# Performance work log

Measured on AMD Instinct MI355X. Metric: run time of the kernel, lower is better.

The kernel has to match this reference:

```python
import jax, jax.numpy as jnp
import numpy as np

H = 4  # attention heads


def gat_layer(x, src, dst, W, a_src, a_dst, b, N):
    """PyG-style GATConv (concat=True, negative_slope=0.2, eval-mode dropout)."""
    h = (x @ W).reshape(N, H, -1)                       # [N,H,C]
    es = jnp.einsum('nhc,hc->nh', h, a_src)             # per-node src score
    ed = jnp.einsum('nhc,hc->nh', h, a_dst)             # per-node dst score
    e = jax.nn.leaky_relu(es[src] + ed[dst], negative_slope=0.2)  # [E,H]
    # segment softmax over incoming edges of each destination node
    emax = jax.ops.segment_max(e, dst, num_segments=N)
    ee = jnp.exp(e - emax[dst])
    denom = jax.ops.segment_sum(ee, dst, num_segments=N)
    alpha = ee / (denom[dst] + 1e-16)                   # [E,H]
    out = jax.ops.segment_sum(h[src] * alpha[..., None], dst, num_segments=N)
    return out.reshape(N, -1) + b                        # [N,H*C]


def setup_inputs() -> dict:
    key = jax.random.key(0)
    ks = jax.random.split(key, 13)
    N, E, D, Q = 50000, 800000, 256, 8
    HID, OUT = 256, 256
    Ch, Co = HID // H, OUT // H
    inp = {}
    inp['x'] = jax.random.normal(ks[0], (N, D), dtype=jnp.float32)
    inp['edge_index'] = jax.random.randint(ks[1], (2, E), 0, N, dtype=jnp.int64)
    inp['query_embedding'] = jax.random.normal(ks[2], (Q, OUT), dtype=jnp.float32)
    # layer 1: input_dim -> heads * (hidden_dim//heads)
    inp['W1'] = jax.random.normal(ks[3], (D, HID), dtype=jnp.float32) / np.sqrt(D).astype(np.float32)
    inp['a_src1'] = jax.random.normal(ks[4], (H, Ch), dtype=jnp.float32) / np.sqrt(Ch).astype(np.float32)
    inp['a_dst1'] = jax.random.normal(ks[5], (H, Ch), dtype=jnp.float32) / np.sqrt(Ch).astype(np.float32)
    inp['b1'] = jnp.zeros((HID,), dtype=jnp.float32)
    # layer 2: hidden_dim -> heads * (output_dim//heads)
    inp['W2'] = jax.random.normal(ks[6], (HID, OUT), dtype=jnp.float32) / np.sqrt(HID).astype(np.float32)
    inp['a_src2'] = jax.random.normal(ks[7], (H, Co), dtype=jnp.float32) / np.sqrt(Co).astype(np.float32)
    inp['a_dst2'] = jax.random.normal(ks[8], (H, Co), dtype=jnp.float32) / np.sqrt(Co).astype(np.float32)
    inp['b2'] = jnp.zeros((OUT,), dtype=jnp.float32)
    # node classifier over concat([query, node]) -> 1 (intended Linear(2*OUT, 1))
    inp['Wc'] = jax.random.normal(ks[9], (2 * OUT, 1), dtype=jnp.float32) / np.sqrt(2 * OUT).astype(np.float32)
    inp['bc'] = jnp.zeros((1,), dtype=jnp.float32)
    return inp


def reference(x, edge_index, query_embedding, W1, a_src1, a_dst1, b1,
              W2, a_src2, a_dst2, b2, Wc, bc):
    N = x.shape[0]
    loops = jnp.arange(N, dtype=edge_index.dtype)        # GATConv add_self_loops=True
    src = jnp.concatenate([edge_index[0], loops])
    dst = jnp.concatenate([edge_index[1], loops])
    h = jax.nn.relu(gat_layer(x, src, dst, W1, a_src1, a_dst1, b1, N))
    emb = gat_layer(h, src, dst, W2, a_src2, a_dst2, b2, N)  # [N, OUT]
    D = emb.shape[1]
    # scores[q,n] = Linear(concat(query[q], emb[n])) — computed without
    # materializing the [Q,N,2D] concat (identical math).
    q_part = query_embedding @ Wc[:D] + bc               # [Q,1]
    n_part = emb @ Wc[D:]                                # [N,1]
    node_scores = q_part[:, 0][:, None] + n_part[:, 0][None, :]  # [Q,N]
    return emb, node_scores
```

## Files before the change

kernel.cpp:

```cpp
#include <hip/hip_runtime.h>

typedef unsigned short u16;
typedef unsigned int   u32;
typedef __attribute__((ext_vector_type(8))) short short8v;
typedef __attribute__((ext_vector_type(8))) unsigned short us8;
typedef __attribute__((ext_vector_type(4))) float f32x4;

static __device__ __forceinline__ float bf2f(u16 u){ union{u32 i; float f;} v; v.i=(u32)u<<16; return v.f; }
static __device__ __forceinline__ u16 f2bf(float f){ union{float f; u32 i;} u; u.f=f; u32 r=u.i+0x7FFFu+((u.i>>16)&1u); return (u16)(r>>16); }

static __device__ __forceinline__ float ld1(const void* p, size_t i, int f32){
  return f32 ? ((const float*)p)[i] : bf2f(((const u16*)p)[i]);
}
static __device__ __forceinline__ float4 ld4(const void* p, size_t i, int f32){
  if (f32) return *((const float4*)((const float*)p + i));
  ushort4 v = *((const ushort4*)((const u16*)p + i));
  return make_float4(bf2f(v.x), bf2f(v.y), bf2f(v.z), bf2f(v.w));
}
static __device__ __forceinline__ void st4(void* p, size_t i, float4 v, int f32){
  if (f32) *((float4*)((float*)p + i)) = v;
  else { ushort4 o; o.x=f2bf(v.x); o.y=f2bf(v.y); o.z=f2bf(v.z); o.w=f2bf(v.w); *((ushort4*)((u16*)p + i)) = o; }
}
static __device__ __forceinline__ void st1(void* p, size_t i, float v, int f32){
  if (f32) ((float*)p)[i] = v; else ((u16*)p)[i] = f2bf(v);
}
static __device__ __forceinline__ int lde(const int* ei, size_t i, int i64){
  return i64 ? ei[2*i] : ei[i];
}
static __device__ __forceinline__ int clampi(int v, int lo, int hi){ return v<lo?lo:(v>hi?hi:v); }

__global__ void detect_kernel(const u32* __restrict__ x, const int* __restrict__ ei,
                              int* __restrict__ flags){
  __shared__ int cnt[2];
  int t = threadIdx.x;
  if (t < 2) cnt[t] = 0;
  __syncthreads();
  int good = 0;
  for (int i = t; i < 4096; i += 256){
    u32 e = (x[i] >> 7) & 0xFFu;
    if (e >= 90u && e <= 150u) good++;
  }
  atomicAdd(&cnt[0], good);
  int nzodd = 0;
  for (int i = t; i < 2048; i += 256){
    if (ei[2*i+1] != 0) nzodd++;
  }
  atomicAdd(&cnt[1], nzodd);
  __syncthreads();
  if (t == 0){
    flags[0] = (cnt[0] < 2867) ? 1 : 0;
    flags[1] = (cnt[1] == 0) ? 1 : 0;
  }
}

__global__ void count_kernel(const int* __restrict__ ei, int E, int N,
                             int* __restrict__ deg, const int* __restrict__ flags){
  int i64 = flags[1];
  int i = blockIdx.x*blockDim.x + threadIdx.x;
  int Et = E + N;
  if (i < Et){
    int d = (i < E) ? clampi(lde(ei, (size_t)E + i, i64), 0, N-1) : (i - E);
    atomicAdd(&deg[d], 1);
  }
}

__global__ __launch_bounds__(256) void scan1_kernel(const int* __restrict__ deg,
    int* __restrict__ offs, int* __restrict__ bsum, int N){
  __shared__ int sm[256];
  int t = threadIdx.x;
  int i = blockIdx.x*256 + t;
  int v = (i < N) ? deg[i] : 0;
  sm[t] = v; __syncthreads();
  #pragma unroll
  for (int off = 1; off < 256; off <<= 1){
    int u = (t >= off) ? sm[t-off] : 0;
    __syncthreads();
    sm[t] += u;
    __syncthreads();
  }
  if (i < N) offs[i] = sm[t] - v;
  if (t == 255) bsum[blockIdx.x] = sm[255];
}

__global__ __launch_bounds__(1024) void scan2_kernel(const int* __restrict__ bsum,
    int* __restrict__ bpre, int NB){
  __shared__ int sm[1024];
  int t = threadIdx.x;
  int v = (t < NB) ? bsum[t] : 0;
  sm[t] = v; __syncthreads();
  #pragma unroll
  for (int off = 1; off < 1024; off <<= 1){
    int u = (t >= off) ? sm[t-off] : 0;
    __syncthreads();
    sm[t] += u;
    __syncthreads();
  }
  if (t < NB) bpre[t] = sm[t] - v;
  if (t == 1023) bpre[NB] = sm[1023];
}

__global__ __launch_bounds__(256) void scan3_kernel(int* __restrict__ offs,
    int* __restrict__ cursor, const int* __restrict__ bpre, int N, int NB){
  int i = blockIdx.x*256 + threadIdx.x;
  if (i < N){
    int v = offs[i] + bpre[blockIdx.x];
    offs[i] = v; cursor[i] = v;
  }
  if (i == 0) offs[N] = bpre[NB];
}

__global__ void scatter_kernel(const int* __restrict__ ei, int E, int N,
    int* __restrict__ cursor, int* __restrict__ csr_src, const int* __restrict__ flags){
  int i64 = flags[1];
  int i = blockIdx.x*blockDim.x + threadIdx.x;
  int Et = E + N;
  if (i < Et){
    int s, d;
    if (i < E){
      s = clampi(lde(ei, i, i64), 0, N-1);
      d = clampi(lde(ei, (size_t)E + i, i64), 0, N-1);
    } else { s = i - E; d = s; }
    int p = atomicAdd(&cursor[d], 1);
    csr_src[p] = s;
  }
}

__global__ __launch_bounds__(256) void gemm_mfma(const void* __restrict__ A,
    const void* __restrict__ B, u16* __restrict__ C, int M, int aIsInput,
    const int* __restrict__ flags){
  int af32 = aIsInput ? flags[0] : 0;
  int bf32 = flags[0];
  __shared__ __align__(16) u16 As[128][40];
  __shared__ __align__(16) u16 Bt[64][264];
  int tid = threadIdx.x;
  int col0 = blockIdx.x * 64;
  int row0 = blockIdx.y * 128;

  {
    int k = tid;
    if (bf32){
      const float* Bp = (const float*)B + (size_t)k*256 + col0;
      #pragma unroll
      for (int j = 0; j < 64; j += 4){
        float4 v = *(const float4*)(Bp + j);
        Bt[j+0][k] = f2bf(v.x); Bt[j+1][k] = f2bf(v.y);
        Bt[j+2][k] = f2bf(v.z); Bt[j+3][k] = f2bf(v.w);
      }
    } else {
      const u16* Bp = (const u16*)B + (size_t)k*256 + col0;
      #pragma unroll
      for (int j = 0; j < 64; j += 4){
        ushort4 v = *(const ushort4*)(Bp + j);
        Bt[j+0][k] = v.x; Bt[j+1][k] = v.y; Bt[j+2][k] = v.z; Bt[j+3][k] = v.w;
      }
    }
  }

  int wave = tid >> 6, lane = tid & 63;
  int wm = wave >> 1, wn = wave & 1;
  int l15 = lane & 15, l4 = lane >> 4;
  f32x4 acc[4][2] = {};
  int arow = tid >> 1, akseg = (tid & 1) * 16;

  for (int k0 = 0; k0 < 256; k0 += 32){
    __syncthreads();
    {
      int gr = row0 + arow;
      us8 p0 = (us8){0,0,0,0,0,0,0,0}, p1 = (us8){0,0,0,0,0,0,0,0};
      if (gr < M){
        if (af32){
          const float* Ap = (const float*)A + (size_t)gr*256 + k0 + akseg;
          float4 a0 = *(const float4*)(Ap+0), a1 = *(const float4*)(Ap+4);
          float4 a2 = *(const float4*)(Ap+8), a3 = *(const float4*)(Ap+12);
          p0 = (us8){f2bf(a0.x),f2bf(a0.y),f2bf(a0.z),f2bf(a0.w),
                     f2bf(a1.x),f2bf(a1.y),f2bf(a1.z),f2bf(a1.w)};
          p1 = (us8){f2bf(a2.x),f2bf(a2.y),f2bf(a2.z),f2bf(a2.w),
                     f2bf(a3.x),f2bf(a3.y),f2bf(a3.z),f2bf(a3.w)};
        } else {
          const u16* Ap = (const u16*)A + (size_t)gr*256 + k0 + akseg;
          p0 = *(const us8*)Ap; p1 = *(const us8*)(Ap+8);
        }
      }
      *(us8*)&As[arow][akseg]   = p0;
      *(us8*)&As[arow][akseg+8] = p1;
    }
    __syncthreads();
    short8v a[4], b[2];
    #pragma unroll
    for (int mi = 0; mi < 4; mi++)
      a[mi] = *(const short8v*)&As[wm*64 + mi*16 + l15][8*l4];
    #pragma unroll
    for (int ni = 0; ni < 2; ni++)
      b[ni] = *(const short8v*)&Bt[wn*32 + ni*16 + l15][k0 + 8*l4];
    #pragma unroll
    for (int mi = 0; mi < 4; mi++)
      #pragma unroll
      for (int ni = 0; ni < 2; ni++)
        acc[mi][ni] = __builtin_amdgcn_mfma_f32_16x16x32_bf16(a[mi], b[ni], acc[mi][ni], 0, 0, 0);
  }

  #pragma unroll
  for (int mi = 0; mi < 4; mi++){
    #pragma unroll
    for (int ni = 0; ni < 2; ni++){
      #pragma unroll
      for (int r = 0; r < 4; r++){
        int row = row0 + wm*64 + mi*16 + l4*4 + r;
        int col = col0 + wn*32 + ni*16 + l15;
        if (row < M) C[(size_t)row*256 + col] = f2bf(acc[mi][ni][r]);
      }
    }
  }
}

__global__ __launch_bounds__(256) void scores_kernel(const u16* __restrict__ h,
    const void* __restrict__ a_src, const void* __restrict__ a_dst,
    float* __restrict__ es, float* __restrict__ ed, int N, const int* __restrict__ flags){
  int f32 = flags[0];
  int ln = threadIdx.x & 63;
  int n = blockIdx.x*4 + (threadIdx.x >> 6);
  if (n >= N) return;
  int c0 = ln*4, hd = ln >> 4;
  ushort4 hv = *(const ushort4*)&h[(size_t)n*256 + c0];
  float4 s4 = ld4(a_src, c0, f32);
  float4 d4 = ld4(a_dst, c0, f32);
  float ps = bf2f(hv.x)*s4.x + bf2f(hv.y)*s4.y + bf2f(hv.z)*s4.z + bf2f(hv.w)*s4.w;
  float pd = bf2f(hv.x)*d4.x + bf2f(hv.y)*d4.y + bf2f(hv.z)*d4.z + bf2f(hv.w)*d4.w;
  #pragma unroll
  for (int off = 1; off < 16; off <<= 1){
    ps += __shfl_xor(ps, off, 64);
    pd += __shfl_xor(pd, off, 64);
  }
  if ((ln & 15) == 0){ es[(size_t)n*4 + hd] = ps; ed[(size_t)n*4 + hd] = pd; }
}

__global__ __launch_bounds__(256) void agg_kernel(const u16* __restrict__ h,
    const int* __restrict__ csr_src, const int* __restrict__ offs,
    const float* __restrict__ es, const float* __restrict__ ed, int N,
    const void* __restrict__ bias, void* __restrict__ out, int do_relu, int outIsOutput,
    const int* __restrict__ flags){
  int f32in = flags[0];
  int of32  = outIsOutput ? flags[0] : 0;
  int ln = threadIdx.x & 63;
  int n = blockIdx.x*4 + (threadIdx.x >> 6);
  if (n >= N) return;
  int beg = offs[n], end = offs[n+1];
  int hd = ln >> 4, c0 = ln*4;
  float edn = ed[(size_t)n*4 + hd];
  float a0=0.f, a1=0.f, a2=0.f, a3=0.f, ws=0.f;
  int i = beg;
  for (; i + 8 <= end; i += 8){
    int s[8]; float x[8]; ushort4 hv[8];
    #pragma unroll
    for (int j = 0; j < 8; j++) s[j] = csr_src[i+j];
    #pragma unroll
    for (int j = 0; j < 8; j++) x[j] = es[(size_t)s[j]*4 + hd];
    #pragma unroll
    for (int j = 0; j < 8; j++) hv[j] = *(const ushort4*)&h[(size_t)s[j]*256 + c0];
    #pragma unroll
    for (int j = 0; j < 8; j++){
      float t = x[j] + edn; t = (t > 0.f) ? t : 0.2f*t; t = fminf(t, 60.f);
      float w = __expf(t);
      a0 += w*bf2f(hv[j].x); a1 += w*bf2f(hv[j].y);
      a2 += w*bf2f(hv[j].z); a3 += w*bf2f(hv[j].w);
      ws += w;
    }
  }
  for (; i + 4 <= end; i += 4){
    int s[4]; float x[4]; ushort4 hv[4];
    #pragma unroll
    for (int j = 0; j < 4; j++) s[j] = csr_src[i+j];
    #pragma unroll
    for (int j = 0; j < 4; j++) x[j] = es[(size_t)s[j]*4 + hd];
    #pragma unroll
    for (int j = 0; j < 4; j++) hv[j] = *(const ushort4*)&h[(size_t)s[j]*256 + c0];
    #pragma unroll
    for (int j = 0; j < 4; j++){
      float t = x[j] + edn; t = (t > 0.f) ? t : 0.2f*t; t = fminf(t, 60.f);
      float w = __expf(t);
      a0 += w*bf2f(hv[j].x); a1 += w*bf2f(hv[j].y);
      a2 += w*bf2f(hv[j].z); a3 += w*bf2f(hv[j].w);
      ws += w;
    }
  }
  for (; i < end; i++){
    int s = csr_src[i];
    float t = es[(size_t)s*4 + hd] + edn; t = (t > 0.f) ? t : 0.2f*t; t = fminf(t, 60.f);
    float w = __expf(t);
    ushort4 hv = *(const ushort4*)&h[(size_t)s*256 + c0];
    a0 += w*bf2f(hv.x); a1 += w*bf2f(hv.y);
    a2 += w*bf2f(hv.z); a3 += w*bf2f(hv.w);
    ws += w;
  }
  float inv = 1.f / (ws + 1e-16f);
  float4 bv = ld4(bias, c0, f32in);
  float4 ov = make_float4(a0*inv + bv.x, a1*inv + bv.y, a2*inv + bv.z, a3*inv + bv.w);
  if (do_relu){
    ov.x = fmaxf(ov.x, 0.f); ov.y = fmaxf(ov.y, 0.f);
    ov.z = fmaxf(ov.z, 0.f); ov.w = fmaxf(ov.w, 0.f);
  }
  st4(out, (size_t)n*256 + c0, ov, of32);
}

__global__ void qpart_kernel(const void* __restrict__ query, const void* __restrict__ Wc,
    const void* __restrict__ bc, float* __restrict__ qp, int Q, const int* __restrict__ flags){
  int f32 = flags[0];
  int q = threadIdx.x >> 5, ln = threadIdx.x & 31;
  if (q >= Q) return;
  float s = 0.f;
  for (int j = ln; j < 256; j += 32) s += ld1(query, q*256 + j, f32) * ld1(Wc, j, f32);
  #pragma unroll
  for (int off = 16; off; off >>= 1) s += __shfl_down(s, off, 32);
  if (ln == 0) qp[q] = s + ld1(bc, 0, f32);
}

__global__ __launch_bounds__(256) void nscore_kernel(const void* __restrict__ dout,
    const void* __restrict__ Wc, const float* __restrict__ qp, int N, int Q,
    const int* __restrict__ flags){
  int f32 = flags[0];
  int wv = threadIdx.x >> 6, ln = threadIdx.x & 63;
  int n = blockIdx.x * 4 + wv;
  if (n >= N) return;
  float4 e4 = ld4(dout, (size_t)n*256 + ln*4, f32);
  float4 w4 = ld4(Wc, 256 + ln*4, f32);
  float v = e4.x*w4.x + e4.y*w4.y + e4.z*w4.z + e4.w*w4.w;
  #pragma unroll
  for (int off = 32; off; off >>= 1) v += __shfl_down(v, off, 64);
  v = __shfl(v, 0, 64);
  if (ln < Q) st1((void*)dout, (size_t)N*256 + (size_t)ln*N + n, qp[ln] + v, f32);
}

extern "C" void kernel_launch(void* const* d_in, const int* in_sizes, int n_in,
                              void* d_out, int out_size, void* d_ws, size_t ws_size,
                              hipStream_t stream){
  const void* x     = d_in[0];
  const int*  ei    = (const int*)d_in[1];
  const void* query = d_in[2];
  const void* W1    = d_in[3];
  const void* as1   = d_in[4];
  const void* ad1   = d_in[5];
  const void* b1    = d_in[6];
  const void* W2    = d_in[7];
  const void* as2   = d_in[8];
  const void* ad2   = d_in[9];
  const void* b2    = d_in[10];
  const void* Wc    = d_in[11];
  const void* bc    = d_in[12];

  int N = in_sizes[0] / 256;
  int E = in_sizes[1] / 2;
  int Q = in_sizes[2] / 256;
  int Et = E + N;
  int NB = (N + 255) / 256;

  char* p = (char*)d_ws;
  auto alloc = [&](size_t bytes)->char*{
    char* r = p; p += (bytes + 255) & ~(size_t)255; return r;
  };
  int*  flags   = (int*) alloc(256);
  u16*  bufA    = (u16*) alloc((size_t)N*256*2);
  u16*  bufB    = (u16*) alloc((size_t)N*256*2);
  float* es     = (float*)alloc((size_t)N*4*4);
  float* ed     = (float*)alloc((size_t)N*4*4);
  int*  deg     = (int*)  alloc((size_t)N*4);
  int*  offs    = (int*)  alloc((size_t)(N+1)*4);
  int*  cursor  = (int*)  alloc((size_t)N*4);
  int*  csr_src = (int*)  alloc((size_t)Et*4);
  int*  bsum    = (int*)  alloc((size_t)(NB+1)*4);
  int*  bpre    = (int*)  alloc((size_t)(NB+1)*4);
  float* qp     = (float*)alloc(64*4);

  const int thr = 256;
  detect_kernel<<<1, 256, 0, stream>>>((const u32*)x, ei, flags);

  hipMemsetAsync(deg, 0, (size_t)N*4, stream);
  count_kernel  <<<(Et + thr-1)/thr, thr, 0, stream>>>(ei, E, N, deg, flags);
  scan1_kernel  <<<NB, 256, 0, stream>>>(deg, offs, bsum, N);
  scan2_kernel  <<<1, 1024, 0, stream>>>(bsum, bpre, NB);
  scan3_kernel  <<<NB, 256, 0, stream>>>(offs, cursor, bpre, N, NB);
  scatter_kernel<<<(Et + thr-1)/thr, thr, 0, stream>>>(ei, E, N, cursor, csr_src, flags);

  dim3 ggrid(4, (N + 127)/128);
  dim3 ngrid((N + 3)/4);
  gemm_mfma    <<<ggrid, 256, 0, stream>>>(x, W1, bufA, N, 1, flags);
  scores_kernel<<<ngrid, 256, 0, stream>>>(bufA, as1, ad1, es, ed, N, flags);
  agg_kernel   <<<ngrid, 256, 0, stream>>>(bufA, csr_src, offs, es, ed, N, b1, bufB, 1, 0, flags);
  gemm_mfma    <<<ggrid, 256, 0, stream>>>(bufB, W2, bufA, N, 0, flags);
  scores_kernel<<<ngrid, 256, 0, stream>>>(bufA, as2, ad2, es, ed, N, flags);
  agg_kernel   <<<ngrid, 256, 0, stream>>>(bufA, csr_src, offs, es, ed, N, b2, d_out, 0, 1, flags);
  qpart_kernel <<<1, 256, 0, stream>>>(query, Wc, bc, qp, Q, flags);
  nscore_kernel<<<ngrid, 256, 0, stream>>>(d_out, Wc, qp, N, Q, flags);
}
```

Measured before the change: 356.0 us.

## Split GAT aggregation across column slices and edge lanes, store byte offsets in CSR

The aggregation kernel now gives each node 8 blocks, one per 32-column slice. Within a wave, 8 lane groups each handle a different edge, and the partial sums are combined with xor shuffles at the end. The CSR array now holds precomputed byte offsets (src*512), so address math is lighter, and the kernel uses nontemporal loads and stores. This exposes more memory-level parallelism for the gather-bound aggregation. In exchange, the per-node offsets, csr entries, and es values are fetched 8 times over, and a shuffle reduction is added.

New measurement: 587.9 us. +65.1%, slower.

```diff
diff --git a/kernel.cpp b/kernel.cpp
--- a/kernel.cpp
+++ b/kernel.cpp
@@ -5,6 +5,7 @@
 typedef __attribute__((ext_vector_type(8))) short short8v;
 typedef __attribute__((ext_vector_type(8))) unsigned short us8;
 typedef __attribute__((ext_vector_type(4))) float f32x4;
+typedef __attribute__((ext_vector_type(2))) unsigned int u32x2;
 
 static __device__ __forceinline__ float bf2f(u16 u){ union{u32 i; float f;} v; v.i=(u32)u<<16; return v.f; }
 static __device__ __forceinline__ u16 f2bf(float f){ union{float f; u32 i;} u; u.f=f; u32 r=u.i+0x7FFFu+((u.i>>16)&1u); return (u16)(r>>16); }
@@ -16,10 +17,6 @@
   if (f32) return *((const float4*)((const float*)p + i));
   ushort4 v = *((const ushort4*)((const u16*)p + i));
   return make_float4(bf2f(v.x), bf2f(v.y), bf2f(v.z), bf2f(v.w));
-}
-static __device__ __forceinline__ void st4(void* p, size_t i, float4 v, int f32){
-  if (f32) *((float4*)((float*)p + i)) = v;
-  else { ushort4 o; o.x=f2bf(v.x); o.y=f2bf(v.y); o.z=f2bf(v.z); o.w=f2bf(v.w); *((ushort4*)((u16*)p + i)) = o; }
 }
 static __device__ __forceinline__ void st1(void* p, size_t i, float v, int f32){
   if (f32) ((float*)p)[i] = v; else ((u16*)p)[i] = f2bf(v);
@@ -110,7 +107,7 @@
 }
 
 __global__ void scatter_kernel(const int* __restrict__ ei, int E, int N,
-    int* __restrict__ cursor, int* __restrict__ csr_src, const int* __restrict__ flags){
+    int* __restrict__ cursor, int* __restrict__ csr_boff, const int* __restrict__ flags){
   int i64 = flags[1];
   int i = blockIdx.x*blockDim.x + threadIdx.x;
   int Et = E + N;
@@ -121,7 +118,7 @@
       d = clampi(lde(ei, (size_t)E + i, i64), 0, N-1);
     } else { s = i - E; d = s; }
     int p = atomicAdd(&cursor[d], 1);
-    csr_src[p] = s;
+    csr_boff[p] = s * 512;
   }
 }
 
@@ -235,71 +232,66 @@
 }
 
 __global__ __launch_bounds__(256) void agg_kernel(const u16* __restrict__ h,
-    const int* __restrict__ csr_src, const int* __restrict__ offs,
+    const int* __restrict__ csr_boff, const int* __restrict__ offs,
     const float* __restrict__ es, const float* __restrict__ ed, int N,
     const void* __restrict__ bias, void* __restrict__ out, int do_relu, int outIsOutput,
     const int* __restrict__ flags){
   int f32in = flags[0];
   int of32  = outIsOutput ? flags[0] : 0;
-  int ln = threadIdx.x & 63;
-  int n = blockIdx.x*4 + (threadIdx.x >> 6);
+  int slice = blockIdx.x & 7;
+  int wv = threadIdx.x >> 6, ln = threadIdx.x & 63;
+  int n = (blockIdx.x >> 3) * 4 + wv;
   if (n >= N) return;
+  int e8 = ln >> 3;
+  int c8 = ln & 7;
+  int hd4 = (slice >> 1) * 4;
+  int cbase = slice*32 + c8*4;
   int beg = offs[n], end = offs[n+1];
-  int hd = ln >> 4, c0 = ln*4;
-  float edn = ed[(size_t)n*4 + hd];
+  float edn = ed[(size_t)n*4 + (slice >> 1)];
   float a0=0.f, a1=0.f, a2=0.f, a3=0.f, ws=0.f;
-  int i = beg;
-  for (; i + 8 <= end; i += 8){
-    int s[8]; float x[8]; ushort4 hv[8];
-    #pragma unroll
-    for (int j = 0; j < 8; j++) s[j] = csr_src[i+j];
-    #pragma unroll
-    for (int j = 0; j < 8; j++) x[j] = es[(size_t)s[j]*4 + hd];
-    #pragma unroll
-    for (int j = 0; j < 8; j++) hv[j] = *(const ushort4*)&h[(size_t)s[j]*256 + c0];
-    #pragma unroll
-    for (int j = 0; j < 8; j++){
-      float t = x[j] + edn; t = (t > 0.f) ? t : 0.2f*t; t = fminf(t, 60.f);
-      float w = __expf(t);
-      a0 += w*bf2f(hv[j].x); a1 += w*bf2f(hv[j].y);
-      a2 += w*bf2f(hv[j].z); a3 += w*bf2f(hv[j].w);
-      ws += w;
-    }
-  }
-  for (; i + 4 <= end; i += 4){
-    int s[4]; float x[4]; ushort4 hv[4];
-    #pragma unroll
-    for (int j = 0; j < 4; j++) s[j] = csr_src[i+j];
-    #pragma unroll
-    for (int j = 0; j < 4; j++) x[j] = es[(size_t)s[j]*4 + hd];
-    #pragma unroll
-    for (int j = 0; j < 4; j++) hv[j] = *(const ushort4*)&h[(size_t)s[j]*256 + c0];
-    #pragma unroll
-    for (int j = 0; j < 4; j++){
-      float t = x[j] + edn; t = (t > 0.f) ? t : 0.2f*t; t = fminf(t, 60.f);
-      float w = __expf(t);
-      a0 += w*bf2f(hv[j].x); a1 += w*bf2f(hv[j].y);
-      a2 += w*bf2f(hv[j].z); a3 += w*bf2f(hv[j].w);
-      ws += w;
-    }
-  }
-  for (; i < end; i++){
-    int s = csr_src[i];
-    float t = es[(size_t)s*4 + hd] + edn; t = (t > 0.f) ? t : 0.2f*t; t = fminf(t, 60.f);
-    float w = __expf(t);
-    ushort4 hv = *(const ushort4*)&h[(size_t)s*256 + c0];
+  const char* hbase = (const char*)h;
+  const char* ebase = (const char*)es;
+  size_t coff = (size_t)cbase*2;
+  #pragma unroll 2
+  for (int i = beg; i < end; i += 8){
+    int idx = i + e8;
+    bool ok = idx < end;
+    int boff = __builtin_nontemporal_load(&csr_boff[ok ? idx : beg]);
+    float x = *(const float*)(ebase + (boff >> 5) + hd4);
+    float t = x + edn; t = (t > 0.f) ? t : 0.2f*t; t = fminf(t, 60.f);
+    float w = ok ? __expf(t) : 0.f;
+    ushort4 hv = *(const ushort4*)(hbase + boff + coff);
     a0 += w*bf2f(hv.x); a1 += w*bf2f(hv.y);
     a2 += w*bf2f(hv.z); a3 += w*bf2f(hv.w);
     ws += w;
   }
-  float inv = 1.f / (ws + 1e-16f);
-  float4 bv = ld4(bias, c0, f32in);
-  float4 ov = make_float4(a0*inv + bv.x, a1*inv + bv.y, a2*inv + bv.z, a3*inv + bv.w);
-  if (do_relu){
-    ov.x = fmaxf(ov.x, 0.f); ov.y = fmaxf(ov.y, 0.f);
-    ov.z = fmaxf(ov.z, 0.f); ov.w = fmaxf(ov.w, 0.f);
-  }
-  st4(out, (size_t)n*256 + c0, ov, of32);
+  #pragma unroll
+  for (int off = 8; off < 64; off <<= 1){
+    a0 += __shfl_xor(a0, off, 64);
+    a1 += __shfl_xor(a1, off, 64);
+    a2 += __shfl_xor(a2, off, 64);
+    a3 += __shfl_xor(a3, off, 64);
+    ws += __shfl_xor(ws, off, 64);
+  }
+  if (e8 == 0){
+    float inv = 1.f / (ws + 1e-16f);
+    float4 bv = ld4(bias, cbase, f32in);
+    float o0 = a0*inv + bv.x, o1 = a1*inv + bv.y;
+    float o2 = a2*inv + bv.z, o3 = a3*inv + bv.w;
+    if (do_relu){
+      o0 = fmaxf(o0, 0.f); o1 = fmaxf(o1, 0.f);
+      o2 = fmaxf(o2, 0.f); o3 = fmaxf(o3, 0.f);
+    }
+    if (of32){
+      f32x4 ov = (f32x4){o0, o1, o2, o3};
+      __builtin_nontemporal_store(ov, (f32x4*)((float*)out + (size_t)n*256 + cbase));
+    } else {
+      u32x2 uv;
+      uv.x = (u32)f2bf(o0) | ((u32)f2bf(o1) << 16);
+      uv.y = (u32)f2bf(o2) | ((u32)f2bf(o3) << 16);
+      __builtin_nontemporal_store(uv, (u32x2*)((u16*)out + (size_t)n*256 + cbase));
+    }
+  }
 }
 
 __global__ void qpart_kernel(const void* __restrict__ query, const void* __restrict__ Wc,
@@ -357,18 +349,18 @@
   auto alloc = [&](size_t bytes)->char*{
     char* r = p; p += (bytes + 255) & ~(size_t)255; return r;
   };
-  int*  flags   = (int*) alloc(256);
-  u16*  bufA    = (u16*) alloc((size_t)N*256*2);
-  u16*  bufB    = (u16*) alloc((size_t)N*256*2);
-  float* es     = (float*)alloc((size_t)N*4*4);
-  float* ed     = (float*)alloc((size_t)N*4*4);
-  int*  deg     = (int*)  alloc((size_t)N*4);
-  int*  offs    = (int*)  alloc((size_t)(N+1)*4);
-  int*  cursor  = (int*)  alloc((size_t)N*4);
-  int*  csr_src = (int*)  alloc((size_t)Et*4);
-  int*  bsum    = (int*)  alloc((size_t)(NB+1)*4);
-  int*  bpre    = (int*)  alloc((size_t)(NB+1)*4);
-  float* qp     = (float*)alloc(64*4);
+  int*  flags    = (int*) alloc(256);
+  u16*  bufA     = (u16*) alloc((size_t)N*256*2);
+  u16*  bufB     = (u16*) alloc((size_t)N*256*2);
+  float* es      = (float*)alloc((size_t)N*4*4);
+  float* ed      = (float*)alloc((size_t)N*4*4);
+  int*  deg      = (int*)  alloc((size_t)N*4);
+  int*  offs     = (int*)  alloc((size_t)(N+1)*4);
+  int*  cursor   = (int*)  alloc((size_t)N*4);
+  int*  csr_boff = (int*)  alloc((size_t)Et*4);
+  int*  bsum     = (int*)  alloc((size_t)(NB+1)*4);
+  int*  bpre     = (int*)  alloc((size_t)(NB+1)*4);
+  float* qp      = (float*)alloc(64*4);
 
   const int thr = 256;
   detect_kernel<<<1, 256, 0, stream>>>((const u32*)x, ei, flags);
@@ -378,16 +370,17 @@
   scan1_kernel  <<<NB, 256, 0, stream>>>(deg, offs, bsum, N);
   scan2_kernel  <<<1, 1024, 0, stream>>>(bsum, bpre, NB);
   scan3_kernel  <<<NB, 256, 0, stream>>>(offs, cursor, bpre, N, NB);
-  scatter_kernel<<<(Et + thr-1)/thr, thr, 0, stream>>>(ei, E, N, cursor, csr_src, flags);
+  scatter_kernel<<<(Et + thr-1)/thr, thr, 0, stream>>>(ei, E, N, cursor, csr_boff, flags);
 
   dim3 ggrid(4, (N + 127)/128);
   dim3 ngrid((N + 3)/4);
+  dim3 agrid(8 * ((N + 3)/4));
   gemm_mfma    <<<ggrid, 256, 0, stream>>>(x, W1, bufA, N, 1, flags);
   scores_kernel<<<ngrid, 256, 0, stream>>>(bufA, as1, ad1, es, ed, N, flags);
-  agg_kernel   <<<ngrid, 256, 0, stream>>>(bufA, csr_src, offs, es, ed, N, b1, bufB, 1, 0, flags);
+  agg_kernel   <<<agrid, 256, 0, stream>>>(bufA, csr_boff, offs, es, ed, N, b1, bufB, 1, 0, flags);
   gemm_mfma    <<<ggrid, 256, 0, stream>>>(bufB, W2, bufA, N, 0, flags);
   scores_kernel<<<ngrid, 256, 0, stream>>>(bufA, as2, ad2, es, ed, N, flags);
-  agg_kernel   <<<ngrid, 256, 0, stream>>>(bufA, csr_src, offs, es, ed, N, b2, d_out, 0, 1, flags);
+  agg_kernel   <<<agrid, 256, 0, stream>>>(bufA, csr_boff, offs, es, ed, N, b2, d_out, 0, 1, flags);
   qpart_kernel <<<1, 256, 0, stream>>>(query, Wc, bc, qp, Q, flags);
   nscore_kernel<<<ngrid, 256, 0, stream>>>(d_out, Wc, qp, N, Q, flags);
 }
```

## Pretranspose weights and preconvert x, drop LDS staging in MFMA GEMM

Applied to the files above, without the earlier changes.

Adds a small kernel that transposes and converts each weight matrix to bf16 once, and a kernel that converts fp32 x to bf16 up front. The GEMM then loads A and B fragments straight from global memory into MFMA operands, with no shared-memory staging and no __syncthreads. This removes the per-block transpose of the full B slice and the per-tile barriers. In exchange it adds an extra pass over x, and each wave re-reads A and B from global or L2 memory instead of sharing them through LDS.

New measurement: 384.7 us. 1.08x slower.

```diff
diff --git a/kernel.cpp b/kernel.cpp
--- a/kernel.cpp
+++ b/kernel.cpp
@@ -125,80 +125,63 @@
   }
 }
 
-__global__ __launch_bounds__(256) void gemm_mfma(const void* __restrict__ A,
-    const void* __restrict__ B, u16* __restrict__ C, int M, int aIsInput,
-    const int* __restrict__ flags){
-  int af32 = aIsInput ? flags[0] : 0;
-  int bf32 = flags[0];
-  __shared__ __align__(16) u16 As[128][40];
-  __shared__ __align__(16) u16 Bt[64][264];
+__global__ __launch_bounds__(256) void btrans_kernel(const void* __restrict__ B,
+    u16* __restrict__ BT, const int* __restrict__ flags){
+  int f32 = flags[0];
+  __shared__ u16 tile[64][65];
+  int k0 = blockIdx.y*64, c0 = blockIdx.x*64;
+  int r0 = threadIdx.x >> 6, c = threadIdx.x & 63;
+  for (int r = r0; r < 64; r += 4)
+    tile[r][c] = f32 ? f2bf(((const float*)B)[(size_t)(k0+r)*256 + c0 + c])
+                     : ((const u16*)B)[(size_t)(k0+r)*256 + c0 + c];
+  __syncthreads();
+  for (int j = r0; j < 64; j += 4)
+    BT[(size_t)(c0+j)*256 + k0 + c] = tile[c][j];
+}
+
+__global__ __launch_bounds__(256) void convx_kernel(const void* __restrict__ x,
+    u16* __restrict__ out, int N, const int* __restrict__ flags){
+  if (!flags[0]) return;
+  size_t i = (size_t)blockIdx.x*256 + threadIdx.x;
+  if (i*8 >= (size_t)N*256) return;
+  const float* xf = (const float*)x + i*8;
+  float4 v0 = *(const float4*)xf, v1 = *(const float4*)(xf+4);
+  us8 o = (us8){f2bf(v0.x),f2bf(v0.y),f2bf(v0.z),f2bf(v0.w),
+                f2bf(v1.x),f2bf(v1.y),f2bf(v1.z),f2bf(v1.w)};
+  *(us8*)(out + i*8) = o;
+}
+
+__global__ __launch_bounds__(256) void gemm_mfma(const u16* __restrict__ A0,
+    const u16* __restrict__ A1, const u16* __restrict__ BT, u16* __restrict__ C,
+    int M, const int* __restrict__ flags){
+  const u16* A = flags[0] ? A1 : A0;
   int tid = threadIdx.x;
-  int col0 = blockIdx.x * 64;
-  int row0 = blockIdx.y * 128;
-
-  {
-    int k = tid;
-    if (bf32){
-      const float* Bp = (const float*)B + (size_t)k*256 + col0;
-      #pragma unroll
-      for (int j = 0; j < 64; j += 4){
-        float4 v = *(const float4*)(Bp + j);
-        Bt[j+0][k] = f2bf(v.x); Bt[j+1][k] = f2bf(v.y);
-        Bt[j+2][k] = f2bf(v.z); Bt[j+3][k] = f2bf(v.w);
-      }
-    } else {
-      const u16* Bp = (const u16*)B + (size_t)k*256 + col0;
-      #pragma unroll
-      for (int j = 0; j < 64; j += 4){
-        ushort4 v = *(const ushort4*)(Bp + j);
-        Bt[j+0][k] = v.x; Bt[j+1][k] = v.y; Bt[j+2][k] = v.z; Bt[j+3][k] = v.w;
-      }
-    }
-  }
-
   int wave = tid >> 6, lane = tid & 63;
   int wm = wave >> 1, wn = wave & 1;
   int l15 = lane & 15, l4 = lane >> 4;
+  int row0 = blockIdx.y * 128, col0 = blockIdx.x * 64;
+  int arow[4];
+  #pragma unroll
+  for (int mi = 0; mi < 4; mi++)
+    arow[mi] = min(row0 + wm*64 + mi*16 + l15, M-1);
+  const u16* Ab = A + 8*l4;
+  const u16* Bb = BT + (size_t)(col0 + wn*32 + l15)*256 + 8*l4;
   f32x4 acc[4][2] = {};
-  int arow = tid >> 1, akseg = (tid & 1) * 16;
-
+  #pragma unroll 2
   for (int k0 = 0; k0 < 256; k0 += 32){
-    __syncthreads();
-    {
-      int gr = row0 + arow;
-      us8 p0 = (us8){0,0,0,0,0,0,0,0}, p1 = (us8){0,0,0,0,0,0,0,0};
-      if (gr < M){
-        if (af32){
-          const float* Ap = (const float*)A + (size_t)gr*256 + k0 + akseg;
-          float4 a0 = *(const float4*)(Ap+0), a1 = *(const float4*)(Ap+4);
-          float4 a2 = *(const float4*)(Ap+8), a3 = *(const float4*)(Ap+12);
-          p0 = (us8){f2bf(a0.x),f2bf(a0.y),f2bf(a0.z),f2bf(a0.w),
-                     f2bf(a1.x),f2bf(a1.y),f2bf(a1.z),f2bf(a1.w)};
-          p1 = (us8){f2bf(a2.x),f2bf(a2.y),f2bf(a2.z),f2bf(a2.w),
-                     f2bf(a3.x),f2bf(a3.y),f2bf(a3.z),f2bf(a3.w)};
-        } else {
-          const u16* Ap = (const u16*)A + (size_t)gr*256 + k0 + akseg;
-          p0 = *(const us8*)Ap; p1 = *(const us8*)(Ap+8);
-        }
-      }
-      *(us8*)&As[arow][akseg]   = p0;
-      *(us8*)&As[arow][akseg+8] = p1;
-    }
-    __syncthreads();
     short8v a[4], b[2];
     #pragma unroll
     for (int mi = 0; mi < 4; mi++)
-      a[mi] = *(const short8v*)&As[wm*64 + mi*16 + l15][8*l4];
+      a[mi] = *(const short8v*)(Ab + (size_t)arow[mi]*256 + k0);
     #pragma unroll
     for (int ni = 0; ni < 2; ni++)
-      b[ni] = *(const short8v*)&Bt[wn*32 + ni*16 + l15][k0 + 8*l4];
+      b[ni] = *(const short8v*)(Bb + (size_t)ni*16*256 + k0);
     #pragma unroll
     for (int mi = 0; mi < 4; mi++)
       #pragma unroll
       for (int ni = 0; ni < 2; ni++)
         acc[mi][ni] = __builtin_amdgcn_mfma_f32_16x16x32_bf16(a[mi], b[ni], acc[mi][ni], 0, 0, 0);
   }
-
   #pragma unroll
   for (int mi = 0; mi < 4; mi++){
     #pragma unroll
@@ -368,6 +351,8 @@
   int*  csr_src = (int*)  alloc((size_t)Et*4);
   int*  bsum    = (int*)  alloc((size_t)(NB+1)*4);
   int*  bpre    = (int*)  alloc((size_t)(NB+1)*4);
+  u16*  BT1     = (u16*)  alloc(256*256*2);
+  u16*  BT2     = (u16*)  alloc(256*256*2);
   float* qp     = (float*)alloc(64*4);
 
   const int thr = 256;
@@ -380,12 +365,19 @@
   scan3_kernel  <<<NB, 256, 0, stream>>>(offs, cursor, bpre, N, NB);
   scatter_kernel<<<(Et + thr-1)/thr, thr, 0, stream>>>(ei, E, N, cursor, csr_src, flags);
 
+  dim3 tgrid(4, 4);
   dim3 ggrid(4, (N + 127)/128);
   dim3 ngrid((N + 3)/4);
-  gemm_mfma    <<<ggrid, 256, 0, stream>>>(x, W1, bufA, N, 1, flags);
+  int cxblocks = (int)(((size_t)N*256/8 + 255) / 256);
+
+  btrans_kernel<<<tgrid, 256, 0, stream>>>(W1, BT1, flags);
+  btrans_kernel<<<tgrid, 256, 0, stream>>>(W2, BT2, flags);
+  convx_kernel <<<cxblocks, 256, 0, stream>>>(x, bufB, N, flags);
+
+  gemm_mfma    <<<ggrid, 256, 0, stream>>>((const u16*)x, bufB, BT1, bufA, N, flags);
   scores_kernel<<<ngrid, 256, 0, stream>>>(bufA, as1, ad1, es, ed, N, flags);
   agg_kernel   <<<ngrid, 256, 0, stream>>>(bufA, csr_src, offs, es, ed, N, b1, bufB, 1, 0, flags);
-  gemm_mfma    <<<ggrid, 256, 0, stream>>>(bufB, W2, bufA, N, 0, flags);
+  gemm_mfma    <<<ggrid, 256, 0, stream>>>(bufB, bufB, BT2, bufA, N, flags);
   scores_kernel<<<ngrid, 256, 0, stream>>>(bufA, as2, ad2, es, ed, N, flags);
   agg_kernel   <<<ngrid, 256, 0, stream>>>(bufA, csr_src, offs, es, ed, N, b2, d_out, 0, 1, flags);
   qpart_kernel <<<1, 256, 0, stream>>>(query, Wc, bc, qp, Q, flags);
```
